# Kernel optimization log

Hardware: AMD Instinct MI355X
Metric: run time of the kernel (lower is better)

Reference implementation:

```python
import jax, jax.numpy as jnp
import numpy as np

NUM_HEADS = 8


def _nearest_idx(x, x_grid):
    # x: [b,n,dx]; x_grid: [b,H,W,dx] regular grid -> flat nearest cell index [b,n]
    b = x.shape[0]
    H, W = x_grid.shape[1], x_grid.shape[2]
    gf = x_grid.reshape(b, H * W, -1)
    lo = gf[:, :1]   # min corner [b,1,dx]
    hi = gf[:, -1:]  # max corner [b,1,dx]
    dims = jnp.asarray([H, W], dtype=x.dtype)
    t = (x - lo) / (hi - lo) * (dims - 1.0)
    idx = jnp.clip(jnp.round(t), 0.0, dims - 1.0).astype(jnp.int32)  # [b,n,2]
    return idx[..., 0] * W + idx[..., 1]


def _cumcount(idx):
    # per-batch cumulative count of each value, in order of appearance
    b, n = idx.shape
    order = jnp.argsort(idx, axis=1, stable=True)
    s = jnp.take_along_axis(idx, order, axis=1)
    ar = jnp.arange(n)
    new_run = jnp.concatenate([jnp.ones((b, 1), bool), s[:, 1:] != s[:, :-1]], axis=1)
    run_start = jax.lax.cummax(jnp.where(new_run, ar, 0), axis=1)
    cc_sorted = (ar - run_start).astype(jnp.int32)
    return jnp.zeros((b, n), jnp.int32).at[jnp.arange(b)[:, None], order].set(cc_sorted)


def _mhca(q_in, kv, mask, Wq, Wk, Wv, Wo):
    # q_in: [B,1,e]; kv: [B,K,e]; mask: [B,K] (True = attend)
    B, K, e = kv.shape
    dh = e // NUM_HEADS
    q = (q_in @ Wq).reshape(B, 1, NUM_HEADS, dh)
    k = (kv @ Wk).reshape(B, K, NUM_HEADS, dh)
    v = (kv @ Wv).reshape(B, K, NUM_HEADS, dh)
    scores = jnp.einsum('bqhd,bkhd->bhqk', q, k) / jnp.sqrt(jnp.asarray(dh, q.dtype))
    scores = jnp.where(mask[:, None, None, :], scores, jnp.finfo(scores.dtype).min)
    attn = jax.nn.softmax(scores, axis=-1)
    out = jnp.einsum('bhqk,bkhd->bqhd', attn, v).reshape(B, 1, e)
    return out @ Wo


def setup_inputs() -> dict:
    key = jax.random.key(0)
    ks = jax.random.split(key, 8)
    b, n, e, H, W = 8, 8192, 128, 64, 64
    x = jax.random.uniform(ks[0], (b, n, 2), jnp.float32)
    z = jax.random.normal(ks[1], (b, n, e), jnp.float32)
    g0 = jnp.linspace(0.0, 1.0, H)
    g1 = jnp.linspace(0.0, 1.0, W)
    mg = jnp.stack(jnp.meshgrid(g0, g1, indexing='ij'), axis=-1)  # [H,W,2]
    x_grid = jnp.broadcast_to(mg, (b, H, W, 2)).astype(jnp.float32)
    z_grid = jax.random.normal(ks[2], (b, H, W, e), jnp.float32)
    latent = jax.random.normal(ks[3], (e,), jnp.float32)
    scale = 1.0 / np.sqrt(e).astype(np.float32)
    Wq = jax.random.normal(ks[4], (e, e), jnp.float32) * scale
    Wk = jax.random.normal(ks[5], (e, e), jnp.float32) * scale
    Wv = jax.random.normal(ks[6], (e, e), jnp.float32) * scale
    Wo = jax.random.normal(ks[7], (e, e), jnp.float32) * scale
    return {"x": x, "z": z, "x_grid": x_grid, "z_grid": z_grid, "latent": latent,
            "Wq": Wq, "Wk": Wk, "Wv": Wv, "Wo": Wo, "max_patch": 20}


def reference(x, z, x_grid, z_grid, latent, Wq, Wk, Wv, Wo, max_patch):
    b, n, e = z.shape
    H, W = x_grid.shape[1], x_grid.shape[2]
    S = H * W
    nearest = _nearest_idx(x, x_grid)                    # [b,n]
    cc = _cumcount(nearest)                              # [b,n]
    bidx = jnp.broadcast_to(jnp.arange(b)[:, None], (b, n))
    valid = cc < max_patch
    slot = jnp.where(valid, cc, 0)
    # ragged scatter: pack each point's z into its grid cell's padded sequence
    joint = jnp.zeros((b, S, max_patch, e), z.dtype)
    joint = joint.at[bidx, nearest, slot].add(z * valid[..., None].astype(z.dtype))
    zg_flat = z_grid.reshape(b, S, e)
    joint = jnp.concatenate([joint, zg_flat[:, :, None, :]], axis=2)  # [b,S,P+1,e]
    counts = jnp.zeros((b, S), jnp.int32).at[bidx, nearest].add(1)
    mask = jnp.arange(max_patch + 1)[None, None, :] < jnp.minimum(counts, max_patch)[..., None]
    mask = mask.at[..., -1].set(True)  # grid token always attended
    joint = joint.reshape(b * S, max_patch + 1, e)
    mask = mask.reshape(b * S, max_patch + 1)
    q = jnp.broadcast_to(latent, (b * S, 1, e))          # z0_grid queries
    zg = _mhca(q, joint, mask, Wq, Wk, Wv, Wo)           # [b*S,1,e]
    zg = zg.reshape(b, H, W, e)
    return x_grid, zg
```

## Files before the change

### kernel.cpp

```cpp
#include <hip/hip_runtime.h>
#include <cstdint>
#include <cstddef>

#define S_CELLS 4096
#define NB      8
#define NPTS    8192
#define E       128
#define MAXP    20
#define NHEADS  8
#define NPT_ROWS 65536
#define NGR_ROWS 32768

#define WS_COUNTS 0
#define WS_SLOTS  131072
#define WS_WT1    2752512
#define WS_WT2    2793472
#define WS_SC     2828288
#define WS_V      5974016

typedef __attribute__((ext_vector_type(8))) short bf16x8;
typedef __attribute__((ext_vector_type(4))) float f32x4;

__device__ __forceinline__ unsigned short f2bf_bits(float f) {
    unsigned u = __float_as_uint(f);
    unsigned rounded = u + 0x7FFFu + ((u >> 16) & 1u);
    return (unsigned short)(rounded >> 16);
}
__device__ __forceinline__ unsigned short f2bf_rta(float f) {
    return (unsigned short)((__float_as_uint(f) + 0x8000u) >> 16);
}
__device__ __forceinline__ unsigned pack_bf2(float a, float b) {
    unsigned ua = __float_as_uint(a) + 0x8000u;
    unsigned ub = __float_as_uint(b) + 0x8000u;
    return (ua >> 16) | (ub & 0xFFFF0000u);
}
__device__ __forceinline__ float bf2f(unsigned short u) {
    return __uint_as_float(((unsigned)u) << 16);
}

__global__ void __launch_bounds__(256)
k_prep(const float* __restrict__ latent,
       const float* __restrict__ Wq,
       const float* __restrict__ Wk,
       const float* __restrict__ Wv,
       const float* __restrict__ Wo,
       int* __restrict__ counts,
       unsigned short* __restrict__ WT1,
       unsigned short* __restrict__ WT2) {
    const int t   = threadIdx.x;
    const int blk = blockIdx.x;

    {
        int4* c4 = (int4*)counts;
        for (int idx = blk * 256 + t; idx < 8192; idx += 9 * 256)
            c4[idx] = int4{0, 0, 0, 0};
    }

    if (blk == 0) {
        __shared__ float lat[E];
        __shared__ float qv[E];
        const int j = t & 127;
        if (t < E) lat[t] = latent[t];
        __syncthreads();
        float acc = 0.0f;
        for (int k2 = 0; k2 < E; ++k2) acc += lat[k2] * Wq[k2 * E + j];
        qv[j] = acc;
        __syncthreads();
        const int hb = (t >> 7) * 4;
        for (int h = hb; h < hb + 4; ++h) {
            float a = 0.0f;
            #pragma unroll
            for (int d = 0; d < 16; ++d) a += Wk[j * E + h * 16 + d] * qv[h * 16 + d];
            WT1[(size_t)(128 + h) * 136 + j] = f2bf_bits(a * 0.25f);
        }
        for (int idx = t; idx < 8 * 136; idx += 256) {
            int rr = idx / 136, cc = idx - rr * 136;
            WT1[(size_t)(136 + rr) * 136 + cc] = 0;
        }
        return;
    }

    const float* W = (blk < 5) ? Wv : Wo;
    unsigned short* WT = (blk < 5) ? WT1 : WT2;
    const int n0 = ((blk - 1) & 3) * 32;
    __shared__ float lbuf[128][33];
    #pragma unroll
    for (int it = 0; it < 16; ++it) {
        int k  = (t >> 5) + it * 8;
        int nl = t & 31;
        lbuf[k][nl] = W[(size_t)k * E + n0 + nl];
    }
    __syncthreads();
    for (int idx = t; idx < 32 * 136; idx += 256) {
        int nl = idx / 136, k = idx - nl * 136;
        float v = (k < 128) ? lbuf[k][nl] : 0.0f;
        WT[(size_t)(n0 + nl) * 136 + k] = f2bf_bits(v);
    }
}

__device__ __forceinline__ bf16x8 load_afrag_f32(const float* __restrict__ X,
                                                 int row, int kq, int q) {
    const float4* xr = (const float4*)(X + (size_t)row * E);
    float4 lo = xr[kq * 8 + q * 2];
    float4 hi = xr[kq * 8 + q * 2 + 1];
    unsigned u[4];
    u[0] = pack_bf2(lo.x, lo.y);
    u[1] = pack_bf2(lo.z, lo.w);
    u[2] = pack_bf2(hi.x, hi.y);
    u[3] = pack_bf2(hi.z, hi.w);
    union { unsigned u4[4]; bf16x8 v; } cv;
    cv.u4[0] = u[0]; cv.u4[1] = u[1]; cv.u4[2] = u[2]; cv.u4[3] = u[3];
    return cv.v;
}

__global__ void __launch_bounds__(256)
k_main(const float* __restrict__ x,
       const float* __restrict__ x_grid,
       const float* __restrict__ Xz,
       const float* __restrict__ Xg,
       const unsigned short* __restrict__ WT1g,
       int* __restrict__ counts,
       int* __restrict__ slots,
       unsigned short* __restrict__ V,
       float* __restrict__ SC,
       float* __restrict__ out_xgrid) {
    __shared__ unsigned short W_t[19584];

    const int t = threadIdx.x;

    if (blockIdx.x >= 768) {
        int i = (blockIdx.x - 768) * 256 + t;
        out_xgrid[i] = x_grid[i];
        int b = i >> 13;
        float x0 = x[(size_t)i * 2 + 0];
        float x1 = x[(size_t)i * 2 + 1];
        int i0 = (int)rintf(x0 * 63.0f);
        int i1 = (int)rintf(x1 * 63.0f);
        i0 = min(max(i0, 0), 63);
        i1 = min(max(i1, 0), 63);
        int cell = b * S_CELLS + i0 * 64 + i1;
        int slot = atomicAdd(&counts[cell], 1);
        if (slot < MAXP) slots[(size_t)cell * MAXP + slot] = i & (NPTS - 1);
        return;
    }

    {
        const float4* src = (const float4*)WT1g;
        float4* dst = (float4*)W_t;
        #pragma unroll
        for (int it = 0; it < 10; ++it) {
            int idx = t + it * 256;
            if (idx < 2448) dst[idx] = src[idx];
        }
    }
    __syncthreads();

    const int lane = t & 63;
    const int wv   = t >> 6;
    const int cn   = lane & 15;
    const int q    = lane >> 4;

    const int grow0 = blockIdx.x * 128;
    const float* Xsrc;
    int srow;
    if (blockIdx.x < 512) { Xsrc = Xz; srow = grow0; }
    else                  { Xsrc = Xg; srow = grow0 - NPT_ROWS; }

    f32x4 acc[2][9];
    #pragma unroll
    for (int mt = 0; mt < 2; ++mt)
        #pragma unroll
        for (int nt = 0; nt < 9; ++nt)
            acc[mt][nt] = f32x4{0.0f, 0.0f, 0.0f, 0.0f};

    #pragma unroll
    for (int kq = 0; kq < 4; ++kq) {
        bf16x8 a[2];
        #pragma unroll
        for (int mt = 0; mt < 2; ++mt)
            a[mt] = load_afrag_f32(Xsrc, srow + wv * 32 + mt * 16 + cn, kq, q);
        #pragma unroll
        for (int nt = 0; nt < 9; ++nt) {
            const bf16x8 b = *(const bf16x8*)&W_t[(size_t)(nt * 16 + cn) * 136 + kq * 32 + q * 8];
            #pragma unroll
            for (int mt = 0; mt < 2; ++mt)
                acc[mt][nt] = __builtin_amdgcn_mfma_f32_16x16x32_bf16(
                    a[mt], b, acc[mt][nt], 0, 0, 0);
        }
    }

    #pragma unroll
    for (int mt = 0; mt < 2; ++mt) {
        const int rb = grow0 + wv * 32 + mt * 16 + q * 4;
        #pragma unroll
        for (int nt = 0; nt < 8; ++nt)
            #pragma unroll
            for (int r = 0; r < 4; ++r)
                V[(size_t)(rb + r) * E + nt * 16 + cn] = f2bf_rta(acc[mt][nt][r]);
        if (cn < 8) {
            #pragma unroll
            for (int r = 0; r < 4; ++r)
                SC[(size_t)(rb + r) * NHEADS + cn] = acc[mt][8][r];
        }
    }
}

__global__ void __launch_bounds__(1024)
k_attn_proj(const int* __restrict__ counts,
            const int* __restrict__ slots,
            const float* __restrict__ SC,
            const unsigned short* __restrict__ Vg,
            const unsigned short* __restrict__ WT2g,
            float* __restrict__ zg) {
    __shared__ __align__(16) unsigned short X_s[16][136];
    __shared__ int sl_s[16][MAXP + 4];
    __shared__ int cnt_s[16];

    const int t    = threadIdx.x;
    const int lane = t & 63;
    const int wv   = t >> 6;
    const int cb   = blockIdx.x * 16;
    const int b    = cb >> 12;
    const int base = b * NPTS;
    const int cn   = lane & 15;
    const int q    = lane >> 4;

    if (t < 320) {
        int c = t / MAXP, s = t - c * MAXP;
        sl_s[c][s] = slots[(size_t)cb * MAXP + t];
    } else if (t < 336) {
        cnt_s[t - 320] = counts[cb + (t - 320)];
    } else if (t < 400) {
        int i = t - 336;
        sl_s[i >> 2][MAXP + (i & 3)] = 0;
    }

    bf16x8 bfr[4];
    if (wv < 8) {
        #pragma unroll
        for (int kq = 0; kq < 4; ++kq)
            bfr[kq] = *(const bf16x8*)&WT2g[(size_t)(wv * 16 + cn) * 136 + kq * 32 + q * 8];
    }
    __syncthreads();

    const int cell = cb + wv;
    const int m    = min(cnt_s[wv], MAXP);
    const int h    = lane >> 3;

    size_t r0 = (size_t)(NPT_ROWS + cell);
    float mm = SC[r0 * NHEADS + h];
    float ss = 1.0f;
    unsigned v0 = *(const unsigned*)(Vg + r0 * E + 2 * lane);
    float o0 = bf2f((unsigned short)v0);
    float o1 = bf2f((unsigned short)(v0 >> 16));

    for (int t0 = 0; t0 < m; t0 += 4) {
        float av[4], p0[4], p1[4];
        #pragma unroll
        for (int j = 0; j < 4; ++j) {
            int tt = t0 + j;
            int pt = sl_s[wv][tt];
            bool val = tt < m;
            pt = val ? pt : 0;
            size_t r = (size_t)(base + pt);
            float sa = SC[r * NHEADS + h];
            av[j] = val ? sa : -1e30f;
            unsigned vv = *(const unsigned*)(Vg + r * E + 2 * lane);
            p0[j] = bf2f((unsigned short)vv);
            p1[j] = bf2f((unsigned short)(vv >> 16));
        }
        #pragma unroll
        for (int j = 0; j < 4; ++j) {
            float nm = fmaxf(mm, av[j]);
            float e  = __expf(av[j] - nm);
            float al = __expf(mm - nm);
            ss = ss * al + e;
            o0 = o0 * al + e * p0[j];
            o1 = o1 * al + e * p1[j];
            mm = nm;
        }
    }
    float inv = 1.0f / ss;
    *(unsigned*)&X_s[wv][2 * lane] = pack_bf2(o0 * inv, o1 * inv);
    __syncthreads();

    if (wv < 8) {
        f32x4 acc = f32x4{0.0f, 0.0f, 0.0f, 0.0f};
        #pragma unroll
        for (int kq = 0; kq < 4; ++kq) {
            bf16x8 a = *(const bf16x8*)&X_s[cn][kq * 32 + q * 8];
            acc = __builtin_amdgcn_mfma_f32_16x16x32_bf16(a, bfr[kq], acc, 0, 0, 0);
        }
        #pragma unroll
        for (int r = 0; r < 4; ++r)
            zg[(size_t)(cb + q * 4 + r) * E + wv * 16 + cn] = acc[r];
    }
}

extern "C" void kernel_launch(void* const* d_in, const int* in_sizes, int n_in,
                              void* d_out, int out_size, void* d_ws, size_t ws_size,
                              hipStream_t stream) {
    const float* x      = (const float*)d_in[0];
    const float* z      = (const float*)d_in[1];
    const float* x_grid = (const float*)d_in[2];
    const float* z_grid = (const float*)d_in[3];
    const float* latent = (const float*)d_in[4];
    const float* Wq     = (const float*)d_in[5];
    const float* Wk     = (const float*)d_in[6];
    const float* Wv     = (const float*)d_in[7];
    const float* Wo     = (const float*)d_in[8];

    char* ws = (char*)d_ws;
    int*            counts = (int*)(ws + WS_COUNTS);
    int*            slots  = (int*)(ws + WS_SLOTS);
    unsigned short* WT1    = (unsigned short*)(ws + WS_WT1);
    unsigned short* WT2    = (unsigned short*)(ws + WS_WT2);
    float*          SC     = (float*)(ws + WS_SC);
    unsigned short* V      = (unsigned short*)(ws + WS_V);

    float* out_xgrid = (float*)d_out;
    float* zg        = (float*)d_out + NB * NPTS;

    k_prep<<<9, 256, 0, stream>>>(latent, Wq, Wk, Wv, Wo, counts, WT1, WT2);

    k_main<<<1024, 256, 0, stream>>>(x, x_grid, z, z_grid, WT1,
                                     counts, slots, V, SC, out_xgrid);

    k_attn_proj<<<2048, 1024, 0, stream>>>(counts, slots, SC, V, WT2, zg);
}
```

Measured before the change: 140.5 us.

## Shrink attention blocks to 256 threads with two cells per wave

The attention/projection kernel goes from 1024-thread blocks of 16 cells to 256-thread blocks of 8 cells. Each wave now runs two cells' online softmax interleaved to expose more memory-level parallelism, and the output projection reads Wo fragments directly from global memory with the MFMA rows half-used. Separately, the main GEMM kernel issues its first A-fragment global loads before the shared-memory weight copy and barrier, to overlap that latency. The trade-offs are wasted MFMA rows, extra weight reads per block, and loop work set by the larger of the two cells' counts.

```diff
diff --git a/kernel.cpp b/kernel.cpp
--- a/kernel.cpp
+++ b/kernel.cpp
@@ -98,19 +98,18 @@
     }
 }
 
+__device__ __forceinline__ bf16x8 pack_frag(float4 lo, float4 hi) {
+    union { unsigned u4[4]; bf16x8 v; } cv;
+    cv.u4[0] = pack_bf2(lo.x, lo.y);
+    cv.u4[1] = pack_bf2(lo.z, lo.w);
+    cv.u4[2] = pack_bf2(hi.x, hi.y);
+    cv.u4[3] = pack_bf2(hi.z, hi.w);
+    return cv.v;
+}
 __device__ __forceinline__ bf16x8 load_afrag_f32(const float* __restrict__ X,
                                                  int row, int kq, int q) {
     const float4* xr = (const float4*)(X + (size_t)row * E);
-    float4 lo = xr[kq * 8 + q * 2];
-    float4 hi = xr[kq * 8 + q * 2 + 1];
-    unsigned u[4];
-    u[0] = pack_bf2(lo.x, lo.y);
-    u[1] = pack_bf2(lo.z, lo.w);
-    u[2] = pack_bf2(hi.x, hi.y);
-    u[3] = pack_bf2(hi.z, hi.w);
-    union { unsigned u4[4]; bf16x8 v; } cv;
-    cv.u4[0] = u[0]; cv.u4[1] = u[1]; cv.u4[2] = u[2]; cv.u4[3] = u[3];
-    return cv.v;
+    return pack_frag(xr[kq * 8 + q * 2], xr[kq * 8 + q * 2 + 1]);
 }
 
 __global__ void __launch_bounds__(256)
@@ -144,17 +143,6 @@
         return;
     }
 
-    {
-        const float4* src = (const float4*)WT1g;
-        float4* dst = (float4*)W_t;
-        #pragma unroll
-        for (int it = 0; it < 10; ++it) {
-            int idx = t + it * 256;
-            if (idx < 2448) dst[idx] = src[idx];
-        }
-    }
-    __syncthreads();
-
     const int lane = t & 63;
     const int wv   = t >> 6;
     const int cn   = lane & 15;
@@ -166,6 +154,22 @@
     if (blockIdx.x < 512) { Xsrc = Xz; srow = grow0; }
     else                  { Xsrc = Xg; srow = grow0 - NPT_ROWS; }
 
+    const float4* xr0 = (const float4*)(Xsrc + (size_t)(srow + wv * 32 + cn) * E);
+    const float4* xr1 = (const float4*)(Xsrc + (size_t)(srow + wv * 32 + 16 + cn) * E);
+    float4 e00 = xr0[q * 2], e01 = xr0[q * 2 + 1];
+    float4 e10 = xr1[q * 2], e11 = xr1[q * 2 + 1];
+
+    {
+        const float4* src = (const float4*)WT1g;
+        float4* dst = (float4*)W_t;
+        #pragma unroll
+        for (int it = 0; it < 10; ++it) {
+            int idx = t + it * 256;
+            if (idx < 2448) dst[idx] = src[idx];
+        }
+    }
+    __syncthreads();
+
     f32x4 acc[2][9];
     #pragma unroll
     for (int mt = 0; mt < 2; ++mt)
@@ -176,9 +180,13 @@
     #pragma unroll
     for (int kq = 0; kq < 4; ++kq) {
         bf16x8 a[2];
-        #pragma unroll
-        for (int mt = 0; mt < 2; ++mt)
-            a[mt] = load_afrag_f32(Xsrc, srow + wv * 32 + mt * 16 + cn, kq, q);
+        if (kq == 0) {
+            a[0] = pack_frag(e00, e01);
+            a[1] = pack_frag(e10, e11);
+        } else {
+            a[0] = load_afrag_f32(Xsrc, srow + wv * 32 + cn,      kq, q);
+            a[1] = load_afrag_f32(Xsrc, srow + wv * 32 + 16 + cn, kq, q);
+        }
         #pragma unroll
         for (int nt = 0; nt < 9; ++nt) {
             const bf16x8 b = *(const bf16x8*)&W_t[(size_t)(nt * 16 + cn) * 136 + kq * 32 + q * 8];
@@ -205,7 +213,7 @@
     }
 }
 
-__global__ void __launch_bounds__(1024)
+__global__ void __launch_bounds__(256)
 k_attn_proj(const int* __restrict__ counts,
             const int* __restrict__ slots,
             const float* __restrict__ SC,
@@ -213,87 +221,110 @@
             const unsigned short* __restrict__ WT2g,
             float* __restrict__ zg) {
     __shared__ __align__(16) unsigned short X_s[16][136];
-    __shared__ int sl_s[16][MAXP + 4];
-    __shared__ int cnt_s[16];
+    __shared__ int sl_s[8][MAXP + 4];
+    __shared__ int cnt_s[8];
 
     const int t    = threadIdx.x;
     const int lane = t & 63;
     const int wv   = t >> 6;
-    const int cb   = blockIdx.x * 16;
+    const int cb   = blockIdx.x * 8;
     const int b    = cb >> 12;
     const int base = b * NPTS;
     const int cn   = lane & 15;
     const int q    = lane >> 4;
 
-    if (t < 320) {
+    if (t < 160) {
         int c = t / MAXP, s = t - c * MAXP;
         sl_s[c][s] = slots[(size_t)cb * MAXP + t];
-    } else if (t < 336) {
-        cnt_s[t - 320] = counts[cb + (t - 320)];
-    } else if (t < 400) {
-        int i = t - 336;
+    } else if (t < 168) {
+        cnt_s[t - 160] = counts[cb + (t - 160)];
+    } else if (t < 200) {
+        int i = t - 168;
         sl_s[i >> 2][MAXP + (i & 3)] = 0;
     }
-
-    bf16x8 bfr[4];
-    if (wv < 8) {
-        #pragma unroll
-        for (int kq = 0; kq < 4; ++kq)
-            bfr[kq] = *(const bf16x8*)&WT2g[(size_t)(wv * 16 + cn) * 136 + kq * 32 + q * 8];
-    }
     __syncthreads();
 
-    const int cell = cb + wv;
-    const int m    = min(cnt_s[wv], MAXP);
-    const int h    = lane >> 3;
-
-    size_t r0 = (size_t)(NPT_ROWS + cell);
-    float mm = SC[r0 * NHEADS + h];
-    float ss = 1.0f;
-    unsigned v0 = *(const unsigned*)(Vg + r0 * E + 2 * lane);
-    float o0 = bf2f((unsigned short)v0);
-    float o1 = bf2f((unsigned short)(v0 >> 16));
-
-    for (int t0 = 0; t0 < m; t0 += 4) {
-        float av[4], p0[4], p1[4];
+    const int c0 = 2 * wv, c1 = c0 + 1;
+    const int cell0 = cb + c0, cell1 = cb + c1;
+    const int m0 = min(cnt_s[c0], MAXP);
+    const int m1 = min(cnt_s[c1], MAXP);
+    const int h  = lane >> 3;
+
+    size_t g0 = (size_t)(NPT_ROWS + cell0);
+    size_t g1 = (size_t)(NPT_ROWS + cell1);
+    float mmA = SC[g0 * NHEADS + h];
+    float mmB = SC[g1 * NHEADS + h];
+    float ssA = 1.0f, ssB = 1.0f;
+    unsigned vA = *(const unsigned*)(Vg + g0 * E + 2 * lane);
+    unsigned vB = *(const unsigned*)(Vg + g1 * E + 2 * lane);
+    float oA0 = bf2f((unsigned short)vA), oA1 = bf2f((unsigned short)(vA >> 16));
+    float oB0 = bf2f((unsigned short)vB), oB1 = bf2f((unsigned short)(vB >> 16));
+
+    const int mmx = max(m0, m1);
+    for (int t0 = 0; t0 < mmx; t0 += 4) {
+        float avA[4], pA0[4], pA1[4];
+        float avB[4], pB0[4], pB1[4];
         #pragma unroll
         for (int j = 0; j < 4; ++j) {
             int tt = t0 + j;
-            int pt = sl_s[wv][tt];
-            bool val = tt < m;
-            pt = val ? pt : 0;
-            size_t r = (size_t)(base + pt);
-            float sa = SC[r * NHEADS + h];
-            av[j] = val ? sa : -1e30f;
-            unsigned vv = *(const unsigned*)(Vg + r * E + 2 * lane);
-            p0[j] = bf2f((unsigned short)vv);
-            p1[j] = bf2f((unsigned short)(vv >> 16));
+            int ptA = sl_s[c0][tt];
+            int ptB = sl_s[c1][tt];
+            bool vlA = tt < m0, vlB = tt < m1;
+            ptA = vlA ? ptA : 0;
+            ptB = vlB ? ptB : 0;
+            size_t rA = (size_t)(base + ptA);
+            size_t rB = (size_t)(base + ptB);
+            float sA = SC[rA * NHEADS + h];
+            float sB = SC[rB * NHEADS + h];
+            avA[j] = vlA ? sA : -1e30f;
+            avB[j] = vlB ? sB : -1e30f;
+            unsigned wA = *(const unsigned*)(Vg + rA * E + 2 * lane);
+            unsigned wB = *(const unsigned*)(Vg + rB * E + 2 * lane);
+            pA0[j] = bf2f((unsigned short)wA); pA1[j] = bf2f((unsigned short)(wA >> 16));
+            pB0[j] = bf2f((unsigned short)wB); pB1[j] = bf2f((unsigned short)(wB >> 16));
         }
         #pragma unroll
         for (int j = 0; j < 4; ++j) {
-            float nm = fmaxf(mm, av[j]);
-            float e  = __expf(av[j] - nm);
-            float al = __expf(mm - nm);
-            ss = ss * al + e;
-            o0 = o0 * al + e * p0[j];
-            o1 = o1 * al + e * p1[j];
-            mm = nm;
-        }
-    }
-    float inv = 1.0f / ss;
-    *(unsigned*)&X_s[wv][2 * lane] = pack_bf2(o0 * inv, o1 * inv);
+            float nmA = fmaxf(mmA, avA[j]);
+            float eA  = __expf(avA[j] - nmA);
+            float alA = __expf(mmA - nmA);
+            ssA = ssA * alA + eA;
+            oA0 = oA0 * alA + eA * pA0[j];
+            oA1 = oA1 * alA + eA * pA1[j];
+            mmA = nmA;
+            float nmB = fmaxf(mmB, avB[j]);
+            float eB  = __expf(avB[j] - nmB);
+            float alB = __expf(mmB - nmB);
+            ssB = ssB * alB + eB;
+            oB0 = oB0 * alB + eB * pB0[j];
+            oB1 = oB1 * alB + eB * pB1[j];
+            mmB = nmB;
+        }
+    }
+    float invA = 1.0f / ssA;
+    float invB = 1.0f / ssB;
+    *(unsigned*)&X_s[c0][2 * lane] = pack_bf2(oA0 * invA, oA1 * invA);
+    *(unsigned*)&X_s[c1][2 * lane] = pack_bf2(oB0 * invB, oB1 * invB);
     __syncthreads();
 
-    if (wv < 8) {
-        f32x4 acc = f32x4{0.0f, 0.0f, 0.0f, 0.0f};
+    {
+        f32x4 acc0 = f32x4{0.0f, 0.0f, 0.0f, 0.0f};
+        f32x4 acc1 = f32x4{0.0f, 0.0f, 0.0f, 0.0f};
         #pragma unroll
         for (int kq = 0; kq < 4; ++kq) {
-            bf16x8 a = *(const bf16x8*)&X_s[cn][kq * 32 + q * 8];
-            acc = __builtin_amdgcn_mfma_f32_16x16x32_bf16(a, bfr[kq], acc, 0, 0, 0);
-        }
-        #pragma unroll
-        for (int r = 0; r < 4; ++r)
-            zg[(size_t)(cb + q * 4 + r) * E + wv * 16 + cn] = acc[r];
+            bf16x8 a  = *(const bf16x8*)&X_s[cn][kq * 32 + q * 8];
+            bf16x8 b0 = *(const bf16x8*)&WT2g[(size_t)(wv * 16 + cn) * 136 + kq * 32 + q * 8];
+            bf16x8 b1 = *(const bf16x8*)&WT2g[(size_t)((wv + 4) * 16 + cn) * 136 + kq * 32 + q * 8];
+            acc0 = __builtin_amdgcn_mfma_f32_16x16x32_bf16(a, b0, acc0, 0, 0, 0);
+            acc1 = __builtin_amdgcn_mfma_f32_16x16x32_bf16(a, b1, acc1, 0, 0, 0);
+        }
+        if (q < 2) {
+            #pragma unroll
+            for (int r = 0; r < 4; ++r) {
+                zg[(size_t)(cb + q * 4 + r) * E + wv * 16 + cn]       = acc0[r];
+                zg[(size_t)(cb + q * 4 + r) * E + (wv + 4) * 16 + cn] = acc1[r];
+            }
+        }
     }
 }
 
@@ -326,5 +357,5 @@
     k_main<<<1024, 256, 0, stream>>>(x, x_grid, z, z_grid, WT1,
                                      counts, slots, V, SC, out_xgrid);
 
-    k_attn_proj<<<2048, 1024, 0, stream>>>(counts, slots, SC, V, WT2, zg);
-}
+    k_attn_proj<<<4096, 256, 0, stream>>>(counts, slots, SC, V, WT2, zg);
+}
```

Result: no change. 142.3 us (+1.2%).
